# Performance work log

Hardware: AMD Instinct MI355X
Metric: run time of the kernel (lower is better)

## Reference

```python
import jax, jax.numpy as jnp
import numpy as np

D_MODEL = 1024
HEADS = 16
D_K = D_MODEL // HEADS
D_FF = 4096
EPS = 1e-6


def setup_inputs() -> dict:
    key = jax.random.key(0)
    ks = jax.random.split(key, 20)
    B, S, D = 8, 1024, D_MODEL
    sc = 1.0 / np.sqrt(D)
    scf = 1.0 / np.sqrt(D_FF)
    inp = {
        "x": jax.random.normal(ks[0], (B, S, D), jnp.float32),
        "mask": jnp.ones((B, 1, 1, S), jnp.int32),
        "wq": jax.random.normal(ks[1], (D, D), jnp.float32) * sc,
        "bq": jnp.zeros((D,), jnp.float32),
        "wk": jax.random.normal(ks[2], (D, D), jnp.float32) * sc,
        "bk": jnp.zeros((D,), jnp.float32),
        "wv": jax.random.normal(ks[3], (D, D), jnp.float32) * sc,
        "bv": jnp.zeros((D,), jnp.float32),
        "wo": jax.random.normal(ks[4], (D, D), jnp.float32) * sc,
        "bo": jnp.zeros((D,), jnp.float32),
        "w1": jax.random.normal(ks[5], (D_FF, D), jnp.float32) * sc,
        "b1": jnp.zeros((D_FF,), jnp.float32),
        "w2": jax.random.normal(ks[6], (D, D_FF), jnp.float32) * scf,
        "b2": jnp.zeros((D,), jnp.float32),
        "g1": jnp.ones((D,), jnp.float32),
        "be1": jnp.zeros((D,), jnp.float32),
        "g2": jnp.ones((D,), jnp.float32),
        "be2": jnp.zeros((D,), jnp.float32),
    }
    return inp


def _layernorm(x, gamma, beta):
    # Faithful to custom LayerNorm: unbiased std (ddof=1), divide by (std+eps)
    mean = jnp.mean(x, axis=-1, keepdims=True)
    std = jnp.std(x, axis=-1, ddof=1, keepdims=True)
    return gamma * (x - mean) / (std + EPS) + beta


def _mha(x, mask, wq, bq, wk, bk, wv, bv, wo, bo):
    B, S, D = x.shape
    q = x @ wq.T + bq
    k = x @ wk.T + bk
    v = x @ wv.T + bv
    # [B,S,D] -> [B,H,S,dk]
    q = q.reshape(B, S, HEADS, D_K).transpose(0, 2, 1, 3)
    k = k.reshape(B, S, HEADS, D_K).transpose(0, 2, 1, 3)
    v = v.reshape(B, S, HEADS, D_K).transpose(0, 2, 1, 3)
    scores = jnp.einsum("bhqd,bhkd->bhqk", q, k) / np.sqrt(D_K).astype(np.float32)
    scores = jnp.where(mask == 0, jnp.float32(-1e9), scores)
    attn = jax.nn.softmax(scores, axis=-1)
    out = jnp.einsum("bhqk,bhkd->bhqd", attn, v)
    out = out.transpose(0, 2, 1, 3).reshape(B, S, D)
    return out @ wo.T + bo


def reference(x, mask, wq, bq, wk, bk, wv, bv, wo, bo, w1, b1, w2, b2, g1, be1, g2, be2):
    # residual 1: x + MHA(LN(x))
    h = _layernorm(x, g1, be1)
    x = x + _mha(h, mask, wq, bq, wk, bk, wv, bv, wo, bo)
    # residual 2: x + FFN(LN(x))
    h = _layernorm(x, g2, be2)
    ff = jax.nn.relu(h @ w1.T + b1) @ w2.T + b2
    return x + ff
```

## Files before the change

kernel.cpp:

```cpp
#include <hip/hip_runtime.h>

typedef __attribute__((ext_vector_type(8))) short short8;
typedef __attribute__((ext_vector_type(4))) short short4_t;
typedef __attribute__((ext_vector_type(4))) float floatx4;
typedef __attribute__((ext_vector_type(16))) float floatx16;

#define NTOK 8192
#define S_ 1024
#define DM 1024

__device__ __forceinline__ unsigned short f2b(float f) {
    union { float f; unsigned u; } v; v.f = f;
    unsigned r = v.u + 0x7FFF + ((v.u >> 16) & 1);
    return (unsigned short)(r >> 16);
}

__device__ __forceinline__ float b2f(unsigned short u) {
    union { unsigned u; float f; } v; v.u = ((unsigned)u) << 16;
    return v.f;
}

__device__ __forceinline__ void gl_lds16(const void* g, void* l) {
    __builtin_amdgcn_global_load_lds((const __attribute__((address_space(1))) void*)g,
                                     (__attribute__((address_space(3))) void*)l, 16, 0, 0);
}

__global__ __launch_bounds__(256) void prep_kernel(const float* __restrict__ wq,
                                                   const float* __restrict__ wk,
                                                   const float* __restrict__ wv,
                                                   const float* __restrict__ wo,
                                                   const float* __restrict__ w1,
                                                   const float* __restrict__ w2,
                                                   const float* __restrict__ bq,
                                                   const float* __restrict__ bk,
                                                   const float* __restrict__ bv,
                                                   const int* __restrict__ mask,
                                                   const float* __restrict__ x,
                                                   const float* __restrict__ g1,
                                                   const float* __restrict__ be1,
                                                   unsigned short* __restrict__ wqkv_bf,
                                                   unsigned short* __restrict__ wo_bf,
                                                   unsigned short* __restrict__ w1_bf,
                                                   unsigned short* __restrict__ w2_bf,
                                                   float* __restrict__ bqkv,
                                                   float* __restrict__ mbias,
                                                   int* __restrict__ mflags,
                                                   unsigned short* __restrict__ h_bf) {
    const int bid = blockIdx.x;
    const int t = threadIdx.x;
    if (bid < 12288) {
        const int q = bid * 256 + t;
        const float* src;
        unsigned short* dst;
        int lq;
        if (q < 786432) {
            src = (q < 262144) ? wq : (q < 524288 ? wk : wv);
            lq = q & 262143;
            dst = wqkv_bf + (size_t)(q >> 18) * 1048576;
        } else if (q < 1048576) {
            src = wo; lq = q - 786432; dst = wo_bf;
        } else if (q < 2097152) {
            src = w1; lq = q - 1048576; dst = w1_bf;
        } else {
            src = w2; lq = q - 2097152; dst = w2_bf;
        }
        const float4 v = *reinterpret_cast<const float4*>(src + (size_t)lq * 4);
        short4_t o;
        o.x = (short)f2b(v.x); o.y = (short)f2b(v.y);
        o.z = (short)f2b(v.z); o.w = (short)f2b(v.w);
        *reinterpret_cast<short4_t*>(dst + (size_t)lq * 4) = o;
        return;
    }
    if (bid == 12288) {
#pragma unroll
        for (int it = 0; it < 3; ++it) {
            const int q = t + it * 256;
            const float* src = (q < 256) ? bq : (q < 512 ? bk : bv);
            const int lq = q & 255;
            *reinterpret_cast<float4*>(bqkv + q * 4) =
                *reinterpret_cast<const float4*>(src + lq * 4);
        }
        return;
    }
    if (bid == 12289) {
#pragma unroll
        for (int it = 0; it < 8; ++it) {
            const int q = t + it * 256;
            const int4 m = *reinterpret_cast<const int4*>(mask + q * 4);
            float4 o;
            o.x = (m.x == 0) ? -1e9f : 0.f;
            o.y = (m.y == 0) ? -1e9f : 0.f;
            o.z = (m.z == 0) ? -1e9f : 0.f;
            o.w = (m.w == 0) ? -1e9f : 0.f;
            *reinterpret_cast<float4*>(mbias + q * 4) = o;
        }
        if (t < 128) {
            int f = 0;
            const int* mp = mask + t * 64;
#pragma unroll
            for (int k = 0; k < 64; ++k) f |= (mp[k] == 0) ? 1 : 0;
            mflags[t] = f;
        }
        return;
    }
    const int row = bid - 12290;
    const float4 xv = *reinterpret_cast<const float4*>(x + (size_t)row * DM + t * 4);
    float s = xv.x + xv.y + xv.z + xv.w;
#pragma unroll
    for (int off = 32; off > 0; off >>= 1) s += __shfl_down(s, off);
    __shared__ float red[8];
    const int wid = t >> 6, lane = t & 63;
    if (lane == 0) red[wid] = s;
    __syncthreads();
    const float mean = (red[0] + red[1] + red[2] + red[3]) * (1.f / 1024.f);
    const float dx = xv.x - mean, dy = xv.y - mean, dz = xv.z - mean, dw = xv.w - mean;
    float ss = dx * dx + dy * dy + dz * dz + dw * dw;
#pragma unroll
    for (int off = 32; off > 0; off >>= 1) ss += __shfl_down(ss, off);
    if (lane == 0) red[4 + wid] = ss;
    __syncthreads();
    const float var = (red[4] + red[5] + red[6] + red[7]) * (1.f / 1023.f);
    const float inv = 1.f / (sqrtf(var) + 1e-6f);
    const float4 gv = *reinterpret_cast<const float4*>(g1 + t * 4);
    const float4 bev = *reinterpret_cast<const float4*>(be1 + t * 4);
    short4_t o;
    o.x = (short)f2b(gv.x * dx * inv + bev.x);
    o.y = (short)f2b(gv.y * dy * inv + bev.y);
    o.z = (short)f2b(gv.z * dz * inv + bev.z);
    o.w = (short)f2b(gv.w * dw * inv + bev.w);
    *reinterpret_cast<short4_t*>(h_bf + (size_t)row * DM + t * 4) = o;
}

__global__ __launch_bounds__(256) void ln_bf16(const unsigned short* __restrict__ xb,
                                               const float* __restrict__ g,
                                               const float* __restrict__ be,
                                               unsigned short* __restrict__ out) {
    const int row = blockIdx.x;
    const int t = threadIdx.x;
    const short4_t xv4 = *reinterpret_cast<const short4_t*>(xb + (size_t)row * DM + t * 4);
    float xv[4];
#pragma unroll
    for (int j = 0; j < 4; ++j) xv[j] = b2f((unsigned short)xv4[j]);
    float s = xv[0] + xv[1] + xv[2] + xv[3];
#pragma unroll
    for (int off = 32; off > 0; off >>= 1) s += __shfl_down(s, off);
    __shared__ float red[8];
    const int wid = t >> 6, lane = t & 63;
    if (lane == 0) red[wid] = s;
    __syncthreads();
    const float mean = (red[0] + red[1] + red[2] + red[3]) * (1.f / 1024.f);
    float d[4];
#pragma unroll
    for (int j = 0; j < 4; ++j) d[j] = xv[j] - mean;
    float ss = d[0] * d[0] + d[1] * d[1] + d[2] * d[2] + d[3] * d[3];
#pragma unroll
    for (int off = 32; off > 0; off >>= 1) ss += __shfl_down(ss, off);
    if (lane == 0) red[4 + wid] = ss;
    __syncthreads();
    const float var = (red[4] + red[5] + red[6] + red[7]) * (1.f / 1023.f);
    const float inv = 1.f / (sqrtf(var) + 1e-6f);
    const float4 gv = *reinterpret_cast<const float4*>(g + t * 4);
    const float4 bev = *reinterpret_cast<const float4*>(be + t * 4);
    short4_t o;
    o.x = (short)f2b(gv.x * d[0] * inv + bev.x);
    o.y = (short)f2b(gv.y * d[1] * inv + bev.y);
    o.z = (short)f2b(gv.z * d[2] * inv + bev.z);
    o.w = (short)f2b(gv.w * d[3] * inv + bev.w);
    *reinterpret_cast<short4_t*>(out + (size_t)row * DM + t * 4) = o;
}

template <int EPI>
__global__ __launch_bounds__(256, 2) void gemm_bt(const unsigned short* __restrict__ A,
                                                  const unsigned short* __restrict__ Bm,
                                                  const float* __restrict__ bias,
                                                  const void* __restrict__ res,
                                                  void* __restrict__ outp,
                                                  int M, int N, int K, int tilesX) {
    __shared__ __align__(16) unsigned short lds[2][2][8192];
    const int t = threadIdx.x;
    const int lane = t & 63, wid = t >> 6;
    const int wr = wid >> 1, wc = wid & 1;

    const int bid = blockIdx.x;
    const int xcd = bid & 7;
    const int lid = bid >> 3;
    const int sid = lid >> 5;
    const int off = lid & 31;
    const int gsid = sid * 8 + xcd;
    const int supercols = tilesX >> 2;
    const int srow = gsid / supercols;
    const int scol = gsid - srow * supercols;
    const int rowBase = (srow * 8 + (off >> 2)) * 128;
    const int colBase = (scol * 4 + (off & 3)) * 128;

    const int NT = K >> 6;
    const int lr31 = lane & 31;
    const int kh = lane >> 5;

    const unsigned short* Ag[4];
    const unsigned short* Bg[4];
#pragma unroll
    for (int j = 0; j < 4; ++j) {
        const int L = j * 256 + t;
        const int r = L >> 3;
        const int c = ((L & 7) ^ (r & 7)) * 8;
        Ag[j] = A + (size_t)(rowBase + r) * K + c;
        Bg[j] = Bm + (size_t)(colBase + r) * K + c;
    }

    floatx16 acc[2][2] = {};

#pragma unroll
    for (int j = 0; j < 4; ++j) gl_lds16(Ag[j], &lds[0][0][j * 2048 + wid * 512]);
#pragma unroll
    for (int j = 0; j < 4; ++j) gl_lds16(Bg[j], &lds[0][1][j * 2048 + wid * 512]);
#pragma unroll
    for (int j = 0; j < 4; ++j) { Ag[j] += 64; Bg[j] += 64; }

    int cur = 0;
    for (int tt = 0; tt < NT; ++tt) {
        if (tt + 1 < NT) {
#pragma unroll
            for (int j = 0; j < 4; ++j)
                gl_lds16(Ag[j], &lds[cur ^ 1][0][j * 2048 + wid * 512]);
#pragma unroll
            for (int j = 0; j < 4; ++j)
                gl_lds16(Bg[j], &lds[cur ^ 1][1][j * 2048 + wid * 512]);
#pragma unroll
            for (int j = 0; j < 4; ++j) { Ag[j] += 64; Bg[j] += 64; }
            asm volatile("s_waitcnt vmcnt(8)" ::: "memory");
        } else {
            asm volatile("s_waitcnt vmcnt(0)" ::: "memory");
        }
        __builtin_amdgcn_s_barrier();
        __builtin_amdgcn_sched_barrier(0);
        const unsigned short* Ab = &lds[cur][0][0];
        const unsigned short* Bb = &lds[cur][1][0];
#pragma unroll
        for (int ks = 0; ks < 4; ++ks) {
            short8 af[2], bfr[2];
#pragma unroll
            for (int mf = 0; mf < 2; ++mf) {
                const int r = wr * 64 + mf * 32 + lr31;
                const int cp = (ks * 2 + kh) ^ (r & 7);
                af[mf] = *reinterpret_cast<const short8*>(&Ab[r * 64 + cp * 8]);
            }
#pragma unroll
            for (int nf = 0; nf < 2; ++nf) {
                const int r = wc * 64 + nf * 32 + lr31;
                const int cp = (ks * 2 + kh) ^ (r & 7);
                bfr[nf] = *reinterpret_cast<const short8*>(&Bb[r * 64 + cp * 8]);
            }
            __builtin_amdgcn_s_setprio(1);
#pragma unroll
            for (int mf = 0; mf < 2; ++mf)
#pragma unroll
                for (int nf = 0; nf < 2; ++nf)
                    acc[mf][nf] = __builtin_amdgcn_mfma_f32_32x32x16_bf16(af[mf], bfr[nf], acc[mf][nf], 0, 0, 0);
            __builtin_amdgcn_s_setprio(0);
        }
        __builtin_amdgcn_sched_barrier(0);
        __builtin_amdgcn_s_barrier();
        cur ^= 1;
    }

    const int rbw = rowBase + wr * 64;
    const int cbw = colBase + wc * 64;
    const int lc31 = lane & 31;
    if (EPI == 4) {
        unsigned short* qh = (unsigned short*)outp;
        const float SC2 = 0.18033688f;
#pragma unroll
        for (int nf = 0; nf < 2; ++nf) {
            const int c = cbw + nf * 32 + lc31;
            const float bn = bias[c];
            const int sect = c >> 10;
            const int hh = (c >> 6) & 15;
            const int dd = c & 63;
            const float scl = (sect == 0) ? SC2 : 1.f;
#pragma unroll
            for (int mf = 0; mf < 2; ++mf) {
#pragma unroll
                for (int rg = 0; rg < 4; ++rg) {
                    const int r0 = rbw + mf * 32 + rg * 8 + 4 * kh;
                    const int bb = r0 >> 10, ss = r0 & 1023;
                    if (sect == 2) {
                        short4_t pk;
#pragma unroll
                        for (int j = 0; j < 4; ++j) pk[j] = (short)f2b(acc[mf][nf][rg * 4 + j] + bn);
                        *reinterpret_cast<short4_t*>(
                            &qh[16777216 + ((size_t)((bb * 16 + hh) * 64 + dd)) * 1024 + ss]) = pk;
                    } else {
                        unsigned short* base = qh + sect * 8388608;
#pragma unroll
                        for (int j = 0; j < 4; ++j)
                            base[((size_t)((bb * 16 + hh) * 1024 + ss + j)) * 64 + dd] =
                                f2b((acc[mf][nf][rg * 4 + j] + bn) * scl);
                    }
                }
            }
        }
        return;
    }
#pragma unroll
    for (int nf = 0; nf < 2; ++nf) {
        const int c = cbw + nf * 32 + lc31;
        const float bn = bias[c];
#pragma unroll
        for (int mf = 0; mf < 2; ++mf) {
#pragma unroll
            for (int rg = 0; rg < 4; ++rg) {
#pragma unroll
                for (int j = 0; j < 4; ++j) {
                    const int r = rbw + mf * 32 + rg * 8 + 4 * kh + j;
                    if (EPI == 2) {
                        const float v = acc[mf][nf][rg * 4 + j] + bn +
                                        ((const float*)res)[(size_t)r * N + c];
                        ((unsigned short*)outp)[(size_t)r * N + c] = f2b(v);
                    } else {
                        const float v = acc[mf][nf][rg * 4 + j] + bn +
                                        b2f(((const unsigned short*)res)[(size_t)r * N + c]);
                        ((float*)outp)[(size_t)r * N + c] = v;
                    }
                }
            }
        }
    }
}

__global__ __launch_bounds__(512, 2) void gemm256p(const unsigned short* __restrict__ A,
                                                   const unsigned short* __restrict__ Bm,
                                                   const float* __restrict__ bias,
                                                   unsigned short* __restrict__ outp,
                                                   int M, int N, int K, int tilesX) {
    __shared__ __align__(16) unsigned short Abuf[2][16384];
    __shared__ __align__(16) unsigned short Bbuf[2][16384];
    const int t = threadIdx.x;
    const int lane = t & 63, wid = t >> 6;
    const int wr = wid >> 2, wc = wid & 3;

    const int bid = blockIdx.x;
    const int xcd = bid & 7;
    const int lid = bid >> 3;
    const int sid = lid >> 5;
    const int off = lid & 31;
    const int gsid = sid * 8 + xcd;
    const int supercols = tilesX >> 2;
    const int srow = gsid / supercols;
    const int scol = gsid - srow * supercols;
    const int rowBase = (srow * 8 + (off >> 2)) * 256;
    const int colBase = (scol * 4 + (off & 3)) * 256;

    const int NT = K >> 6;
    const int lr31 = lane & 31;
    const int kh = lane >> 5;
    const int x7 = lane & 7;

    const int rho_s = t >> 3;
    const int csrc = ((t & 7) ^ (rho_s & 7)) * 8;
    const int ldst = t * 8;
    const unsigned short* Bs_[2][2];
    const unsigned short* As_[2][2];
#pragma unroll
    for (int h = 0; h < 2; ++h)
#pragma unroll
        for (int j = 0; j < 2; ++j) {
            const int rr = rho_s + j * 64;
            Bs_[h][j] = Bm + (size_t)(colBase + h * 128 + rr) * K + csrc;
            As_[h][j] = A + (size_t)(rowBase + ((rr >> 6) * 128 + h * 64 + (rr & 63))) * K + csrc;
        }

#define STG_BH(h_, b_, kk_)                                                   \
    do {                                                                      \
        gl_lds16(Bs_[h_][0] + (kk_), &Bbuf[b_][(h_)*8192 + ldst]);            \
        gl_lds16(Bs_[h_][1] + (kk_), &Bbuf[b_][(h_)*8192 + 4096 + ldst]);     \
    } while (0)
#define STG_AH(h_, b_, kk_)                                                   \
    do {                                                                      \
        gl_lds16(As_[h_][0] + (kk_), &Abuf[b_][(h_)*8192 + ldst]);            \
        gl_lds16(As_[h_][1] + (kk_), &Abuf[b_][(h_)*8192 + 4096 + ldst]);     \
    } while (0)

    floatx16 acc[4][2] = {};

    STG_BH(0, 0, 0); STG_BH(1, 0, 0); STG_AH(0, 0, 0); STG_AH(1, 0, 0);
    asm volatile("s_waitcnt vmcnt(0)" ::: "memory");
    __builtin_amdgcn_s_barrier();

    for (int kt = 0; kt < NT; ++kt) {
        const int cur = kt & 1, nxt = cur ^ 1;
        const bool pf = (kt + 1 < NT);
        const int kkn = (pf ? kt + 1 : kt) << 6;
        short8 bfr[2][4];
#pragma unroll
        for (int q = 0; q < 4; ++q) {
            short8 af[4];
            {
                const int rho = wr * 64 + (q & 1) * 32 + lr31;
                const unsigned short* Ab = &Abuf[cur][(q >> 1) * 8192];
#pragma unroll
                for (int s = 0; s < 4; ++s)
                    af[s] = *reinterpret_cast<const short8*>(
                        &Ab[rho * 64 + ((2 * s + kh) ^ x7) * 8]);
            }
            if (q == 0) {
#pragma unroll
                for (int nf = 0; nf < 2; ++nf) {
                    const int gcol = wc * 64 + nf * 32 + lr31;
                    const unsigned short* Bb = &Bbuf[cur][(gcol >> 7) * 8192];
                    const int rho = gcol & 127;
#pragma unroll
                    for (int s = 0; s < 4; ++s)
                        bfr[nf][s] = *reinterpret_cast<const short8*>(
                            &Bb[rho * 64 + ((2 * s + kh) ^ x7) * 8]);
                }
            }
            if (pf) {
                if (q == 0) STG_BH(0, nxt, kkn);
                if (q == 1) STG_BH(1, nxt, kkn);
                if (q == 2) STG_AH(0, nxt, kkn);
                if (q == 3) STG_AH(1, nxt, kkn);
            }
            __builtin_amdgcn_s_barrier();
            asm volatile("s_waitcnt lgkmcnt(0)" ::: "memory");
            __builtin_amdgcn_sched_barrier(0);
            __builtin_amdgcn_s_setprio(1);
#pragma unroll
            for (int s = 0; s < 4; ++s)
#pragma unroll
                for (int nf = 0; nf < 2; ++nf)
                    acc[q][nf] = __builtin_amdgcn_mfma_f32_32x32x16_bf16(af[s], bfr[nf][s], acc[q][nf], 0, 0, 0);
            __builtin_amdgcn_s_setprio(0);
            __builtin_amdgcn_sched_barrier(0);
            if (q == 1) {
                if (pf) asm volatile("s_waitcnt vmcnt(4)" ::: "memory");
                else    asm volatile("s_waitcnt vmcnt(0)" ::: "memory");
            }
            if (q == 3 && pf) asm volatile("s_waitcnt vmcnt(2)" ::: "memory");
            __builtin_amdgcn_s_barrier();
        }
    }
#undef STG_AH
#undef STG_BH

    const int rbw = rowBase + wr * 128;
    const int cbw = colBase + wc * 64;
    const int lc31 = lane & 31;
#pragma unroll
    for (int nf = 0; nf < 2; ++nf) {
        const int c = cbw + nf * 32 + lc31;
        const float bn = bias[c];
#pragma unroll
        for (int q = 0; q < 4; ++q) {
#pragma unroll
            for (int rg = 0; rg < 4; ++rg) {
                const int r0 = rbw + q * 32 + rg * 8 + 4 * kh;
#pragma unroll
                for (int j = 0; j < 4; ++j) {
                    const float v = fmaxf(acc[q][nf][rg * 4 + j] + bn, 0.f);
                    outp[(size_t)(r0 + j) * N + c] = f2b(v);
                }
            }
        }
    }
}

__global__ __launch_bounds__(512) void attn_mfma(const unsigned short* __restrict__ Qh,
                                                 const unsigned short* __restrict__ Kh,
                                                 const unsigned short* __restrict__ Vt,
                                                 const float* __restrict__ mbias,
                                                 const int* __restrict__ mflags,
                                                 unsigned short* __restrict__ out) {
    __shared__ __align__(16) unsigned short Kbuf[2][4096];
    __shared__ __align__(16) unsigned short Vbuf[2][4096];
    __shared__ __align__(16) unsigned short Pbuf[8][16][72];
    const int t = threadIdx.x;
    const int w = t >> 6, l = t & 63;
    const int w4 = w & 3;
    const int g = l >> 4, q16 = l & 15;
    const int x7 = q16 & 7;
    const int bid = blockIdx.x;
    const int swz = (bid & 7) * 128 + (bid >> 3);
    const int bh = swz >> 3, qpair = swz & 7;
    const int qb = qpair * 2 + (w >> 2);
    const int b = bh >> 4, h = bh & 15;

    const size_t qbase = ((size_t)bh * 1024 + qb * 64 + w4 * 16 + q16) * 64;
    const short8 qf0 = *reinterpret_cast<const short8*>(Qh + qbase + g * 8);
    const short8 qf1 = *reinterpret_cast<const short8*>(Qh + qbase + 32 + g * 8);

    const int r0 = t >> 3;
    const int c0 = ((t & 7) ^ (r0 & 7)) * 8;
    const unsigned short* Kg = Kh + (size_t)bh * 65536 + r0 * 64 + c0;
    const unsigned short* Vg = Vt + (size_t)bh * 65536 + r0 * 1024 + c0;
    const float* mbp = mbias + b * 1024;

#define ATTN_STAGE(bi, kc_)                                                        \
    do {                                                                           \
        gl_lds16(Kg + (kc_) * 4096, &Kbuf[bi][w * 512]);                           \
        gl_lds16(Vg + (kc_) * 64, &Vbuf[bi][w * 512]);                             \
    } while (0)

    ATTN_STAGE(0, 0);

    floatx4 oacc[4] = {};
    floatx4 loacc = {};
    short8 ones;
#pragma unroll
    for (int j = 0; j < 8; ++j) ones[j] = (short)0x3F80;

    int cur = 0;
    for (int kc = 0; kc < 16; ++kc) {
        if (kc < 15) {
            ATTN_STAGE(cur ^ 1, kc + 1);
            asm volatile("s_waitcnt vmcnt(2)" ::: "memory");
        } else {
            asm volatile("s_waitcnt vmcnt(0)" ::: "memory");
        }
        __builtin_amdgcn_s_barrier();
        __builtin_amdgcn_sched_barrier(0);
        const unsigned short* Kb = Kbuf[cur];
        const unsigned short* Vb = Vbuf[cur];

        floatx4 st[4] = {};
        __builtin_amdgcn_s_setprio(1);
#pragma unroll
        for (int t4 = 0; t4 < 4; ++t4) {
            const int row = t4 * 16 + q16;
            const short8 kf0 = *reinterpret_cast<const short8*>(&Kb[row * 64 + (g ^ x7) * 8]);
            const short8 kf1 = *reinterpret_cast<const short8*>(&Kb[row * 64 + ((4 + g) ^ x7) * 8]);
            st[t4] = __builtin_amdgcn_mfma_f32_16x16x32_bf16(kf0, qf0, st[t4], 0, 0, 0);
            st[t4] = __builtin_amdgcn_mfma_f32_16x16x32_bf16(kf1, qf1, st[t4], 0, 0, 0);
        }
        __builtin_amdgcn_s_setprio(0);

        if (mflags[b * 16 + kc]) {
#pragma unroll
            for (int t4 = 0; t4 < 4; ++t4) {
                const float4 mbv = *reinterpret_cast<const float4*>(mbp + kc * 64 + t4 * 16 + g * 4);
#pragma unroll
                for (int r = 0; r < 4; ++r) st[t4][r] += ((const float*)&mbv)[r];
            }
        }
#pragma unroll
        for (int t4 = 0; t4 < 4; ++t4) {
            const float p0 = __builtin_exp2f(st[t4][0]);
            const float p1 = __builtin_exp2f(st[t4][1]);
            const float p2 = __builtin_exp2f(st[t4][2]);
            const float p3 = __builtin_exp2f(st[t4][3]);
            unsigned u0, u1;
            asm("v_cvt_pk_bf16_f32 %0, %1, %2" : "=v"(u0) : "v"(p0), "v"(p1));
            asm("v_cvt_pk_bf16_f32 %0, %1, %2" : "=v"(u1) : "v"(p2), "v"(p3));
            uint2 pr; pr.x = u0; pr.y = u1;
            *reinterpret_cast<uint2*>(&Pbuf[w][q16][t4 * 16 + g * 4]) = pr;
        }

        const short8 pf0 = *reinterpret_cast<const short8*>(&Pbuf[w][q16][g * 8]);
        const short8 pf1 = *reinterpret_cast<const short8*>(&Pbuf[w][q16][32 + g * 8]);
        __builtin_amdgcn_s_setprio(1);
        loacc = __builtin_amdgcn_mfma_f32_16x16x32_bf16(pf0, ones, loacc, 0, 0, 0);
        loacc = __builtin_amdgcn_mfma_f32_16x16x32_bf16(pf1, ones, loacc, 0, 0, 0);
#pragma unroll
        for (int n = 0; n < 4; ++n) {
            const int row = n * 16 + q16;
            const short8 vf0 = *reinterpret_cast<const short8*>(&Vb[row * 64 + (g ^ x7) * 8]);
            const short8 vf1 = *reinterpret_cast<const short8*>(&Vb[row * 64 + ((4 + g) ^ x7) * 8]);
            oacc[n] = __builtin_amdgcn_mfma_f32_16x16x32_bf16(pf0, vf0, oacc[n], 0, 0, 0);
            oacc[n] = __builtin_amdgcn_mfma_f32_16x16x32_bf16(pf1, vf1, oacc[n], 0, 0, 0);
        }
        __builtin_amdgcn_s_setprio(0);
        __builtin_amdgcn_sched_barrier(0);
        __builtin_amdgcn_s_barrier();
        cur ^= 1;
    }
#undef ATTN_STAGE

    const size_t obase = ((size_t)b * S_ + qb * 64 + w4 * 16) * 1024 + h * 64;
#pragma unroll
    for (int r = 0; r < 4; ++r) {
        const float invr = 1.f / loacc[r];
        const size_t orow = obase + (size_t)(g * 4 + r) * 1024;
#pragma unroll
        for (int n = 0; n < 4; ++n)
            out[orow + n * 16 + q16] = f2b(oacc[n][r] * invr);
    }
}

extern "C" void kernel_launch(void* const* d_in, const int* in_sizes, int n_in,
                              void* d_out, int out_size, void* d_ws, size_t ws_size,
                              hipStream_t stream) {
    const float* x   = (const float*)d_in[0];
    const int*  mask = (const int*)d_in[1];
    const float* wq  = (const float*)d_in[2];
    const float* bq  = (const float*)d_in[3];
    const float* wk  = (const float*)d_in[4];
    const float* bk  = (const float*)d_in[5];
    const float* wv  = (const float*)d_in[6];
    const float* bv  = (const float*)d_in[7];
    const float* wo  = (const float*)d_in[8];
    const float* bo  = (const float*)d_in[9];
    const float* w1  = (const float*)d_in[10];
    const float* b1  = (const float*)d_in[11];
    const float* w2  = (const float*)d_in[12];
    const float* b2  = (const float*)d_in[13];
    const float* g1  = (const float*)d_in[14];
    const float* be1 = (const float*)d_in[15];
    const float* g2  = (const float*)d_in[16];
    const float* be2 = (const float*)d_in[17];

    char* ws = (char*)d_ws;
    unsigned short* wqkv_bf = (unsigned short*)(ws);
    unsigned short* wo_bf   = (unsigned short*)(ws + 6291456);
    unsigned short* w1_bf   = (unsigned short*)(ws + 8388608);
    unsigned short* w2_bf   = (unsigned short*)(ws + 16777216);
    float*          bqkv    = (float*)(ws + 25165824);
    float*          mbias   = (float*)(ws + 25178112);
    int*            mflags  = (int*)(ws + 25210880);
    unsigned short* h_bf    = (unsigned short*)(ws + 25214976);
    unsigned short* x1b     = (unsigned short*)(ws + 41992192);
    unsigned short* attn_bf = (unsigned short*)(ws + 75546624);
    unsigned short* qkvh    = (unsigned short*)(ws + 92323840);
    unsigned short* ff1_bf  = (unsigned short*)(ws + 92323840);

    prep_kernel<<<20482, 256, 0, stream>>>(wq, wk, wv, wo, w1, w2, bq, bk, bv, mask,
                                           x, g1, be1,
                                           wqkv_bf, wo_bf, w1_bf, w2_bf, bqkv, mbias, mflags, h_bf);

    gemm_bt<4><<<24 * 64, 256, 0, stream>>>(h_bf, wqkv_bf, bqkv, nullptr, qkvh, NTOK, 3072, 1024, 24);
    attn_mfma<<<1024, 512, 0, stream>>>(qkvh, qkvh + 8388608, qkvh + 16777216, mbias, mflags, attn_bf);
    gemm_bt<2><<<8 * 64, 256, 0, stream>>>(attn_bf, wo_bf, bo, x, x1b, NTOK, 1024, 1024, 8);
    ln_bf16<<<NTOK, 256, 0, stream>>>(x1b, g2, be2, h_bf);
    gemm256p<<<512, 512, 0, stream>>>(h_bf, w1_bf, b1, ff1_bf, NTOK, 4096, 1024, 16);
    gemm_bt<5><<<8 * 64, 256, 0, stream>>>(ff1_bf, w2_bf, b2, x1b, (float*)d_out, NTOK, 1024, 4096, 8);
}
```

Before: 346.2 us.

## Single-buffer gemm_bt for higher occupancy and reuse it for FFN1

Drops double buffering in gemm_bt to a single LDS stage, halving shared memory so launch bounds can target four blocks per CU. Latency is meant to be hidden by more resident blocks rather than by in-block prefetch. The dedicated 256x256 pipelined gemm256p kernel for the first FFN matmul is removed and replaced by a new ReLU epilogue variant of gemm_bt with 128x128 tiles. The risk is exposed global-load latency on every k-step, since each step now waits on vmcnt(0) and adds an extra barrier. The smaller tiles for FFN1 also lower data reuse.

```diff
diff --git a/kernel.cpp b/kernel.cpp
--- a/kernel.cpp
+++ b/kernel.cpp
@@ -170,13 +170,13 @@
 }
 
 template <int EPI>
-__global__ __launch_bounds__(256, 2) void gemm_bt(const unsigned short* __restrict__ A,
+__global__ __launch_bounds__(256, 4) void gemm_bt(const unsigned short* __restrict__ A,
                                                   const unsigned short* __restrict__ Bm,
                                                   const float* __restrict__ bias,
                                                   const void* __restrict__ res,
                                                   void* __restrict__ outp,
                                                   int M, int N, int K, int tilesX) {
-    __shared__ __align__(16) unsigned short lds[2][2][8192];
+    __shared__ __align__(16) unsigned short lds[2][8192];
     const int t = threadIdx.x;
     const int lane = t & 63, wid = t >> 6;
     const int wr = wid >> 1, wc = wid & 1;
@@ -210,32 +210,17 @@
 
     floatx16 acc[2][2] = {};
 
-#pragma unroll
-    for (int j = 0; j < 4; ++j) gl_lds16(Ag[j], &lds[0][0][j * 2048 + wid * 512]);
-#pragma unroll
-    for (int j = 0; j < 4; ++j) gl_lds16(Bg[j], &lds[0][1][j * 2048 + wid * 512]);
-#pragma unroll
-    for (int j = 0; j < 4; ++j) { Ag[j] += 64; Bg[j] += 64; }
-
-    int cur = 0;
     for (int tt = 0; tt < NT; ++tt) {
-        if (tt + 1 < NT) {
-#pragma unroll
-            for (int j = 0; j < 4; ++j)
-                gl_lds16(Ag[j], &lds[cur ^ 1][0][j * 2048 + wid * 512]);
-#pragma unroll
-            for (int j = 0; j < 4; ++j)
-                gl_lds16(Bg[j], &lds[cur ^ 1][1][j * 2048 + wid * 512]);
-#pragma unroll
-            for (int j = 0; j < 4; ++j) { Ag[j] += 64; Bg[j] += 64; }
-            asm volatile("s_waitcnt vmcnt(8)" ::: "memory");
-        } else {
-            asm volatile("s_waitcnt vmcnt(0)" ::: "memory");
-        }
+        if (tt > 0) __builtin_amdgcn_s_barrier();
+#pragma unroll
+        for (int j = 0; j < 4; ++j) gl_lds16(Ag[j], &lds[0][j * 2048 + wid * 512]);
+#pragma unroll
+        for (int j = 0; j < 4; ++j) gl_lds16(Bg[j], &lds[1][j * 2048 + wid * 512]);
+#pragma unroll
+        for (int j = 0; j < 4; ++j) { Ag[j] += 64; Bg[j] += 64; }
+        asm volatile("s_waitcnt vmcnt(0)" ::: "memory");
         __builtin_amdgcn_s_barrier();
         __builtin_amdgcn_sched_barrier(0);
-        const unsigned short* Ab = &lds[cur][0][0];
-        const unsigned short* Bb = &lds[cur][1][0];
 #pragma unroll
         for (int ks = 0; ks < 4; ++ks) {
             short8 af[2], bfr[2];
@@ -243,13 +228,13 @@
             for (int mf = 0; mf < 2; ++mf) {
                 const int r = wr * 64 + mf * 32 + lr31;
                 const int cp = (ks * 2 + kh) ^ (r & 7);
-                af[mf] = *reinterpret_cast<const short8*>(&Ab[r * 64 + cp * 8]);
+                af[mf] = *reinterpret_cast<const short8*>(&lds[0][r * 64 + cp * 8]);
             }
 #pragma unroll
             for (int nf = 0; nf < 2; ++nf) {
                 const int r = wc * 64 + nf * 32 + lr31;
                 const int cp = (ks * 2 + kh) ^ (r & 7);
-                bfr[nf] = *reinterpret_cast<const short8*>(&Bb[r * 64 + cp * 8]);
+                bfr[nf] = *reinterpret_cast<const short8*>(&lds[1][r * 64 + cp * 8]);
             }
             __builtin_amdgcn_s_setprio(1);
 #pragma unroll
@@ -260,8 +245,6 @@
             __builtin_amdgcn_s_setprio(0);
         }
         __builtin_amdgcn_sched_barrier(0);
-        __builtin_amdgcn_s_barrier();
-        cur ^= 1;
     }
 
     const int rbw = rowBase + wr * 64;
@@ -317,148 +300,14 @@
                         const float v = acc[mf][nf][rg * 4 + j] + bn +
                                         ((const float*)res)[(size_t)r * N + c];
                         ((unsigned short*)outp)[(size_t)r * N + c] = f2b(v);
+                    } else if (EPI == 3) {
+                        const float v = fmaxf(acc[mf][nf][rg * 4 + j] + bn, 0.f);
+                        ((unsigned short*)outp)[(size_t)r * N + c] = f2b(v);
                     } else {
                         const float v = acc[mf][nf][rg * 4 + j] + bn +
                                         b2f(((const unsigned short*)res)[(size_t)r * N + c]);
                         ((float*)outp)[(size_t)r * N + c] = v;
                     }
-                }
-            }
-        }
-    }
-}
-
-__global__ __launch_bounds__(512, 2) void gemm256p(const unsigned short* __restrict__ A,
-                                                   const unsigned short* __restrict__ Bm,
-                                                   const float* __restrict__ bias,
-                                                   unsigned short* __restrict__ outp,
-                                                   int M, int N, int K, int tilesX) {
-    __shared__ __align__(16) unsigned short Abuf[2][16384];
-    __shared__ __align__(16) unsigned short Bbuf[2][16384];
-    const int t = threadIdx.x;
-    const int lane = t & 63, wid = t >> 6;
-    const int wr = wid >> 2, wc = wid & 3;
-
-    const int bid = blockIdx.x;
-    const int xcd = bid & 7;
-    const int lid = bid >> 3;
-    const int sid = lid >> 5;
-    const int off = lid & 31;
-    const int gsid = sid * 8 + xcd;
-    const int supercols = tilesX >> 2;
-    const int srow = gsid / supercols;
-    const int scol = gsid - srow * supercols;
-    const int rowBase = (srow * 8 + (off >> 2)) * 256;
-    const int colBase = (scol * 4 + (off & 3)) * 256;
-
-    const int NT = K >> 6;
-    const int lr31 = lane & 31;
-    const int kh = lane >> 5;
-    const int x7 = lane & 7;
-
-    const int rho_s = t >> 3;
-    const int csrc = ((t & 7) ^ (rho_s & 7)) * 8;
-    const int ldst = t * 8;
-    const unsigned short* Bs_[2][2];
-    const unsigned short* As_[2][2];
-#pragma unroll
-    for (int h = 0; h < 2; ++h)
-#pragma unroll
-        for (int j = 0; j < 2; ++j) {
-            const int rr = rho_s + j * 64;
-            Bs_[h][j] = Bm + (size_t)(colBase + h * 128 + rr) * K + csrc;
-            As_[h][j] = A + (size_t)(rowBase + ((rr >> 6) * 128 + h * 64 + (rr & 63))) * K + csrc;
-        }
-
-#define STG_BH(h_, b_, kk_)                                                   \
-    do {                                                                      \
-        gl_lds16(Bs_[h_][0] + (kk_), &Bbuf[b_][(h_)*8192 + ldst]);            \
-        gl_lds16(Bs_[h_][1] + (kk_), &Bbuf[b_][(h_)*8192 + 4096 + ldst]);     \
-    } while (0)
-#define STG_AH(h_, b_, kk_)                                                   \
-    do {                                                                      \
-        gl_lds16(As_[h_][0] + (kk_), &Abuf[b_][(h_)*8192 + ldst]);            \
-        gl_lds16(As_[h_][1] + (kk_), &Abuf[b_][(h_)*8192 + 4096 + ldst]);     \
-    } while (0)
-
-    floatx16 acc[4][2] = {};
-
-    STG_BH(0, 0, 0); STG_BH(1, 0, 0); STG_AH(0, 0, 0); STG_AH(1, 0, 0);
-    asm volatile("s_waitcnt vmcnt(0)" ::: "memory");
-    __builtin_amdgcn_s_barrier();
-
-    for (int kt = 0; kt < NT; ++kt) {
-        const int cur = kt & 1, nxt = cur ^ 1;
-        const bool pf = (kt + 1 < NT);
-        const int kkn = (pf ? kt + 1 : kt) << 6;
-        short8 bfr[2][4];
-#pragma unroll
-        for (int q = 0; q < 4; ++q) {
-            short8 af[4];
-            {
-                const int rho = wr * 64 + (q & 1) * 32 + lr31;
-                const unsigned short* Ab = &Abuf[cur][(q >> 1) * 8192];
-#pragma unroll
-                for (int s = 0; s < 4; ++s)
-                    af[s] = *reinterpret_cast<const short8*>(
-                        &Ab[rho * 64 + ((2 * s + kh) ^ x7) * 8]);
-            }
-            if (q == 0) {
-#pragma unroll
-                for (int nf = 0; nf < 2; ++nf) {
-                    const int gcol = wc * 64 + nf * 32 + lr31;
-                    const unsigned short* Bb = &Bbuf[cur][(gcol >> 7) * 8192];
-                    const int rho = gcol & 127;
-#pragma unroll
-                    for (int s = 0; s < 4; ++s)
-                        bfr[nf][s] = *reinterpret_cast<const short8*>(
-                            &Bb[rho * 64 + ((2 * s + kh) ^ x7) * 8]);
-                }
-            }
-            if (pf) {
-                if (q == 0) STG_BH(0, nxt, kkn);
-                if (q == 1) STG_BH(1, nxt, kkn);
-                if (q == 2) STG_AH(0, nxt, kkn);
-                if (q == 3) STG_AH(1, nxt, kkn);
-            }
-            __builtin_amdgcn_s_barrier();
-            asm volatile("s_waitcnt lgkmcnt(0)" ::: "memory");
-            __builtin_amdgcn_sched_barrier(0);
-            __builtin_amdgcn_s_setprio(1);
-#pragma unroll
-            for (int s = 0; s < 4; ++s)
-#pragma unroll
-                for (int nf = 0; nf < 2; ++nf)
-                    acc[q][nf] = __builtin_amdgcn_mfma_f32_32x32x16_bf16(af[s], bfr[nf][s], acc[q][nf], 0, 0, 0);
-            __builtin_amdgcn_s_setprio(0);
-            __builtin_amdgcn_sched_barrier(0);
-            if (q == 1) {
-                if (pf) asm volatile("s_waitcnt vmcnt(4)" ::: "memory");
-                else    asm volatile("s_waitcnt vmcnt(0)" ::: "memory");
-            }
-            if (q == 3 && pf) asm volatile("s_waitcnt vmcnt(2)" ::: "memory");
-            __builtin_amdgcn_s_barrier();
-        }
-    }
-#undef STG_AH
-#undef STG_BH
-
-    const int rbw = rowBase + wr * 128;
-    const int cbw = colBase + wc * 64;
-    const int lc31 = lane & 31;
-#pragma unroll
-    for (int nf = 0; nf < 2; ++nf) {
-        const int c = cbw + nf * 32 + lc31;
-        const float bn = bias[c];
-#pragma unroll
-        for (int q = 0; q < 4; ++q) {
-#pragma unroll
-            for (int rg = 0; rg < 4; ++rg) {
-                const int r0 = rbw + q * 32 + rg * 8 + 4 * kh;
-#pragma unroll
-                for (int j = 0; j < 4; ++j) {
-                    const float v = fmaxf(acc[q][nf][rg * 4 + j] + bn, 0.f);
-                    outp[(size_t)(r0 + j) * N + c] = f2b(v);
                 }
             }
         }
@@ -630,6 +479,6 @@
     attn_mfma<<<1024, 512, 0, stream>>>(qkvh, qkvh + 8388608, qkvh + 16777216, mbias, mflags, attn_bf);
     gemm_bt<2><<<8 * 64, 256, 0, stream>>>(attn_bf, wo_bf, bo, x, x1b, NTOK, 1024, 1024, 8);
     ln_bf16<<<NTOK, 256, 0, stream>>>(x1b, g2, be2, h_bf);
-    gemm256p<<<512, 512, 0, stream>>>(h_bf, w1_bf, b1, ff1_bf, NTOK, 4096, 1024, 16);
+    gemm_bt<3><<<32 * 64, 256, 0, stream>>>(h_bf, w1_bf, b1, nullptr, ff1_bf, NTOK, 4096, 1024, 32);
     gemm_bt<5><<<8 * 64, 256, 0, stream>>>(ff1_bf, w2_bf, b2, x1b, (float*)d_out, NTOK, 1024, 4096, 8);
 }
```

After: 370.1 us. 1.07x slower.
